# Kernel tuning notes

Hardware: AMD Instinct MI355X
Metric: run time of the kernel (lower is better)

## Reference

```python
import jax, jax.numpy as jnp
import numpy as np

N_HEADS = 16
KEY_SIZE = 64
N_INPUTS = 512
B, T = 128, 200


def setup_inputs() -> dict:
    key = jax.random.key(0)
    ks = jax.random.split(key, 6)
    s = 0.02
    return {
        "x": jax.random.normal(ks[0], (B, T, N_INPUTS), dtype=jnp.float32),
        "Wq": jax.random.normal(ks[1], (N_INPUTS, N_HEADS * KEY_SIZE), dtype=jnp.float32) * s,
        "bq": jnp.zeros((N_HEADS * KEY_SIZE,), dtype=jnp.float32),
        "Wk": jax.random.normal(ks[2], (N_INPUTS, N_HEADS * KEY_SIZE), dtype=jnp.float32) * s,
        "bk": jnp.zeros((N_HEADS * KEY_SIZE,), dtype=jnp.float32),
        "Wv": jax.random.normal(ks[3], (N_INPUTS, N_HEADS * N_INPUTS), dtype=jnp.float32) * s,
        "bv": jnp.zeros((N_HEADS * N_INPUTS,), dtype=jnp.float32),
        "Wp": jax.random.normal(ks[4], (N_HEADS * N_INPUTS, N_INPUTS), dtype=jnp.float32) * s,
        "bp": jnp.zeros((N_INPUTS,), dtype=jnp.float32),
    }


def reference(x, Wq, bq, Wk, bk, Wv, bv, Wp, bp):
    Bx, Tx, C = x.shape
    H, K = N_HEADS, KEY_SIZE
    # projections -> (B, H, T, d)
    q = (x @ Wq + bq).reshape(Bx, Tx, H, K).transpose(0, 2, 1, 3)
    k = (x @ Wk + bk).reshape(Bx, Tx, H, K).transpose(0, 2, 1, 3)
    v = (x @ Wv + bv).reshape(Bx, Tx, H, C).transpose(0, 2, 1, 3)
    scale = 1.0 / np.sqrt(K).astype(np.float32)
    scores = jnp.einsum("bhtk,bhsk->bhts", q, k) * scale  # (B,H,T,T)
    causal = jnp.tril(jnp.ones((Tx, Tx), dtype=bool))
    scores = jnp.where(causal[None, None], scores, -jnp.inf)
    att = jax.nn.softmax(scores, axis=-1)  # dropout p=0.0 (eval)
    y = jnp.einsum("bhts,bhsc->bhtc", att, v)  # (B,H,T,C)
    y = y.transpose(0, 2, 1, 3).reshape(Bx, Tx, H * C)
    return (y @ Wp + bp, att)
```

## Files before the change

### kernel.cpp

```cpp
#include <hip/hip_runtime.h>

typedef unsigned short u16;
typedef short v8s __attribute__((ext_vector_type(8)));
typedef float v4f __attribute__((ext_vector_type(4)));

#define DEV __device__ __forceinline__

constexpr int BATCH = 128;
constexpr int T = 200;
constexpr int C = 512;
constexpr int H = 16;
constexpr int BT = BATCH * T;
constexpr int TP = 208;
constexpr int TPK = 224;
constexpr int HK = 1024;
constexpr int HC = 8192;
constexpr float SCALE = 0.125f;

DEV u16 f2b(float x) {
  union { float f; unsigned u; } v; v.f = x;
  unsigned r = v.u + 0x7fffu + ((v.u >> 16) & 1u);
  return (u16)(r >> 16);
}

__global__ void cast_bf16_kernel(const float* __restrict__ in, u16* __restrict__ out, long n4) {
  long i = (long)blockIdx.x * blockDim.x + threadIdx.x;
  long stride = (long)gridDim.x * blockDim.x;
  for (; i < n4; i += stride) {
    float4 v = *(const float4*)(in + i * 4);
    uint2 o;
    o.x = (unsigned)f2b(v.x) | ((unsigned)f2b(v.y) << 16);
    o.y = (unsigned)f2b(v.z) | ((unsigned)f2b(v.w) << 16);
    *(uint2*)(out + i * 4) = o;
  }
}

__global__ void transpose_cast_kernel(const float* __restrict__ in, u16* __restrict__ out,
                                      int R, int Cc, int Rpad, long inBatch, long outBatch) {
  __shared__ float tile[32][33];
  int b = blockIdx.z;
  int c0 = blockIdx.x * 32, r0 = blockIdx.y * 32;
  int tx = threadIdx.x, ty = threadIdx.y;
  const float* ib = in + (long)b * inBatch;
  u16* ob = out + (long)b * outBatch;
  for (int i = ty; i < 32; i += 8) {
    int r = r0 + i, c = c0 + tx;
    tile[i][tx] = (r < R && c < Cc) ? ib[(long)r * Cc + c] : 0.f;
  }
  __syncthreads();
  for (int i = ty; i < 32; i += 8) {
    int c = c0 + i, r = r0 + tx;
    if (c < Cc && r < Rpad) ob[(long)c * Rpad + r] = f2b(tile[tx][i]);
  }
}

__global__ void cvec_init_kernel(const float* __restrict__ bp, float* __restrict__ cvec) {
  int j = threadIdx.x + blockIdx.x * 256;
  if (j < C) cvec[j] = bp[j];
}
__global__ void cvec_kernel(const float* __restrict__ bv, const float* __restrict__ Wp,
                            float* __restrict__ cvec) {
  int j = blockIdx.x * 256 + threadIdx.x;
  int hc0 = blockIdx.y * 256;
  float acc = 0.f;
  for (int i = 0; i < 256; i++) {
    int hc = hc0 + i;
    acc += bv[hc] * Wp[(long)hc * C + j];
  }
  atomicAdd(&cvec[j], acc);
}

template<bool OUT_BF16, bool BIAS, bool ACCUM>
__global__ __launch_bounds__(256) void gemm_nt_kernel(
    const u16* __restrict__ A, long lda, long strideA,
    const u16* __restrict__ Bt, long ldb, long strideB,
    void* __restrict__ Dp, long ldd, long strideD,
    const float* __restrict__ bias, int K, int ntN) {
  __shared__ __align__(16) u16 As[128 * 64];
  __shared__ __align__(16) u16 Bs[128 * 64];
  int bt = blockIdx.y;
  int tn = blockIdx.x % ntN, tm = blockIdx.x / ntN;
  const u16* Ab = A + (long)bt * strideA + (long)tm * 128 * lda;
  const u16* Bb = Bt + (long)bt * strideB + (long)tn * 128 * ldb;
  int tid = threadIdx.x;
  int lane = tid & 63, wave = tid >> 6;
  int r15 = lane & 15, kg = lane >> 4;
  int wm = (wave & 1) * 64, wn = (wave >> 1) * 64;
  v4f acc[4][4] = {};
  for (int kt = 0; kt < K; kt += 64) {
    uint4 va[4], vb[4];
    #pragma unroll
    for (int i = 0; i < 4; i++) {
      int c = i * 256 + tid;
      long row = c >> 3; int c8 = (c & 7) * 8;
      va[i] = *(const uint4*)(Ab + row * lda + kt + c8);
      vb[i] = *(const uint4*)(Bb + row * ldb + kt + c8);
    }
    __syncthreads();
    #pragma unroll
    for (int i = 0; i < 4; i++) {
      int c = i * 256 + tid;
      *(uint4*)(As + c * 8) = va[i];
      *(uint4*)(Bs + c * 8) = vb[i];
    }
    __syncthreads();
    #pragma unroll
    for (int ks = 0; ks < 2; ks++) {
      v8s af[4], bf_[4];
      int ko = ks * 32 + kg * 8;
      #pragma unroll
      for (int mi = 0; mi < 4; mi++) af[mi] = *(const v8s*)(As + (wm + mi * 16 + r15) * 64 + ko);
      #pragma unroll
      for (int ni = 0; ni < 4; ni++) bf_[ni] = *(const v8s*)(Bs + (wn + ni * 16 + r15) * 64 + ko);
      #pragma unroll
      for (int mi = 0; mi < 4; mi++)
        #pragma unroll
        for (int ni = 0; ni < 4; ni++)
          acc[mi][ni] = __builtin_amdgcn_mfma_f32_16x16x32_bf16(af[mi], bf_[ni], acc[mi][ni], 0, 0, 0);
    }
    __syncthreads();
  }
  #pragma unroll
  for (int mi = 0; mi < 4; mi++) {
    #pragma unroll
    for (int ni = 0; ni < 4; ni++) {
      int colg = tn * 128 + wn + ni * 16 + r15;
      float bb = BIAS ? bias[colg] : 0.f;
      #pragma unroll
      for (int r = 0; r < 4; r++) {
        long rowg = (long)tm * 128 + wm + mi * 16 + kg * 4 + r;
        long off = (long)bt * strideD + rowg * ldd + colg;
        float v = acc[mi][ni][r] + bb;
        if (OUT_BF16)      ((u16*)Dp)[off] = f2b(v);
        else if (ACCUM)    ((float*)Dp)[off] += v;
        else               ((float*)Dp)[off] = v;
      }
    }
  }
}

__global__ __launch_bounds__(256) void attn_kernel(
    const u16* __restrict__ qb, const u16* __restrict__ kb, float* __restrict__ att) {
  __shared__ __align__(16) u16 Qs[TP * 64];
  __shared__ __align__(16) u16 Ks[TP * 64];
  int bh = blockIdx.x;
  int b = bh >> 4, h = bh & 15;
  int tid = threadIdx.x;
  const u16* qg = qb + (long)b * T * HK + h * 64;
  const u16* kg_ = kb + (long)b * T * HK + h * 64;
  for (int c = tid; c < TP * 8; c += 256) {
    long row = c >> 3; int c8 = (c & 7) * 8;
    long srow = row < T ? row : (T - 1);
    *(uint4*)(Qs + c * 8) = *(const uint4*)(qg + srow * HK + c8);
    *(uint4*)(Ks + c * 8) = *(const uint4*)(kg_ + srow * HK + c8);
  }
  __syncthreads();
  int lane = tid & 63, wave = tid >> 6;
  int r15 = lane & 15, kg4 = lane >> 4;
  float* attb = att + (long)bh * T * T;
  for (int tt = wave; tt < 13; tt += 4) {
    v8s aq0 = *(const v8s*)(Qs + (tt * 16 + r15) * 64 + kg4 * 8);
    v8s aq1 = *(const v8s*)(Qs + (tt * 16 + r15) * 64 + 32 + kg4 * 8);
    float sc[13][4];
    #pragma unroll
    for (int j = 0; j < 13; j++) {
      if (j <= tt) {
        v8s bk0 = *(const v8s*)(Ks + (j * 16 + r15) * 64 + kg4 * 8);
        v8s bk1 = *(const v8s*)(Ks + (j * 16 + r15) * 64 + 32 + kg4 * 8);
        v4f a_ = {};
        a_ = __builtin_amdgcn_mfma_f32_16x16x32_bf16(aq0, bk0, a_, 0, 0, 0);
        a_ = __builtin_amdgcn_mfma_f32_16x16x32_bf16(aq1, bk1, a_, 0, 0, 0);
        #pragma unroll
        for (int r = 0; r < 4; r++) {
          int t_ = tt * 16 + kg4 * 4 + r;
          int s_ = j * 16 + r15;
          sc[j][r] = (s_ <= t_) ? a_[r] * SCALE : -__builtin_inff();
        }
      } else {
        #pragma unroll
        for (int r = 0; r < 4; r++) sc[j][r] = -__builtin_inff();
      }
    }
    float sm[4];
    #pragma unroll
    for (int r = 0; r < 4; r++) {
      float m = sc[0][r];
      #pragma unroll
      for (int j = 1; j < 13; j++) m = fmaxf(m, sc[j][r]);
      #pragma unroll
      for (int off = 1; off < 16; off <<= 1) m = fmaxf(m, __shfl_xor(m, off));
      float s = 0.f;
      #pragma unroll
      for (int j = 0; j < 13; j++) { float p = __expf(sc[j][r] - m); sc[j][r] = p; s += p; }
      #pragma unroll
      for (int off = 1; off < 16; off <<= 1) s += __shfl_xor(s, off);
      sm[r] = 1.f / s;
    }
    #pragma unroll
    for (int j = 0; j < 13; j++) {
      int s_ = j * 16 + r15;
      if (s_ < T) {
        #pragma unroll
        for (int r = 0; r < 4; r++) {
          int t_ = tt * 16 + kg4 * 4 + r;
          if (t_ < T) attb[(long)t_ * T + s_] = sc[j][r] * sm[r];
        }
      }
    }
  }
}

__global__ __launch_bounds__(256) void z_kernel(
    const float* __restrict__ att, const u16* __restrict__ xbT,
    u16* __restrict__ zb, int h0, int nhc) {
  __shared__ __align__(16) u16 As_[64 * 32];
  __shared__ __align__(16) u16 Bs_[128 * 32];
  int tt = blockIdx.x & 3, ny = blockIdx.x >> 2;
  int b = blockIdx.y / nhc, hh = blockIdx.y % nhc;
  int h = h0 + hh;
  const float* ab = att + (long)(b * H + h) * T * T;
  const u16* xg = xbT + (long)b * C * TPK;
  int tid = threadIdx.x;
  int lane = tid & 63, wave = tid >> 6;
  int r15 = lane & 15, kg4 = lane >> 4;
  int wm = (wave & 1) * 32, wn = (wave >> 1) * 64;
  v4f acc[2][4] = {};
  int ksteps = (tt + 1) * 2; if (ksteps > 7) ksteps = 7;
  int arow = tid >> 2, ac8 = (tid & 3) * 8;
  for (int ks = 0; ks < ksteps; ks++) {
    int s0 = ks * 32;
    int t_ = tt * 64 + arow;
    __align__(16) u16 tmp[8];
    #pragma unroll
    for (int e = 0; e < 8; e++) {
      int s_ = s0 + ac8 + e;
      float v = (t_ < T && s_ < T) ? ab[(long)t_ * T + s_] : 0.f;
      tmp[e] = f2b(v);
    }
    int c0 = tid, c1 = 256 + tid;
    uint4 bv0 = *(const uint4*)(xg + (long)(ny * 128 + (c0 >> 2)) * TPK + s0 + (c0 & 3) * 8);
    uint4 bv1 = *(const uint4*)(xg + (long)(ny * 128 + (c1 >> 2)) * TPK + s0 + (c1 & 3) * 8);
    __syncthreads();
    *(uint4*)(As_ + arow * 32 + ac8) = *(uint4*)tmp;
    *(uint4*)(Bs_ + c0 * 8) = bv0;
    *(uint4*)(Bs_ + c1 * 8) = bv1;
    __syncthreads();
    int ko = kg4 * 8;
    v8s a0 = *(const v8s*)(As_ + (wm + r15) * 32 + ko);
    v8s a1 = *(const v8s*)(As_ + (wm + 16 + r15) * 32 + ko);
    v8s bf_[4];
    #pragma unroll
    for (int ni = 0; ni < 4; ni++) bf_[ni] = *(const v8s*)(Bs_ + (wn + ni * 16 + r15) * 32 + ko);
    #pragma unroll
    for (int ni = 0; ni < 4; ni++) {
      acc[0][ni] = __builtin_amdgcn_mfma_f32_16x16x32_bf16(a0, bf_[ni], acc[0][ni], 0, 0, 0);
      acc[1][ni] = __builtin_amdgcn_mfma_f32_16x16x32_bf16(a1, bf_[ni], acc[1][ni], 0, 0, 0);
    }
  }
  long ldz = (long)nhc * C;
  #pragma unroll
  for (int mi = 0; mi < 2; mi++) {
    #pragma unroll
    for (int ni = 0; ni < 4; ni++) {
      int i_ = ny * 128 + wn + ni * 16 + r15;
      #pragma unroll
      for (int r = 0; r < 4; r++) {
        int t_ = tt * 64 + wm + mi * 16 + kg4 * 4 + r;
        if (t_ < T) zb[(long)(b * T + t_) * ldz + (long)hh * C + i_] = f2b(acc[mi][ni][r]);
      }
    }
  }
}

extern "C" void kernel_launch(void* const* d_in, const int* in_sizes, int n_in,
                              void* d_out, int out_size, void* d_ws, size_t ws_size,
                              hipStream_t stream) {
  const float* x  = (const float*)d_in[0];
  const float* Wq = (const float*)d_in[1];
  const float* bq = (const float*)d_in[2];
  const float* Wk = (const float*)d_in[3];
  const float* bk = (const float*)d_in[4];
  const float* Wv = (const float*)d_in[5];
  const float* bv = (const float*)d_in[6];
  const float* Wp = (const float*)d_in[7];
  const float* bp = (const float*)d_in[8];
  float* out = (float*)d_out;
  float* att = out + (long)BT * C;

  char* w = (char*)d_ws;
  auto alloc = [&](size_t bytes) -> char* {
    char* p = w; w += (bytes + 255) & ~(size_t)255; return p;
  };
  u16* xb  = (u16*)alloc((size_t)BT * C * 2);
  u16* xbT = (u16*)alloc((size_t)BATCH * C * TPK * 2);
  u16* qb  = (u16*)alloc((size_t)BT * HK * 2);
  u16* kb  = (u16*)alloc((size_t)BT * HK * 2);
  u16* wqT = (u16*)alloc((size_t)HK * C * 2);
  u16* wkT = (u16*)alloc((size_t)HK * C * 2);
  u16* wvb = (u16*)alloc((size_t)C * HC * 2);
  u16* wpT = (u16*)alloc((size_t)C * HC * 2);
  u16* w2t = (u16*)alloc((size_t)C * HC * 2);
  float* cv = (float*)alloc(C * 4);
  size_t used = (size_t)(w - (char*)d_ws);
  size_t rem = ws_size > used ? ws_size - used : 0;
  int nhc = 16;
  while (nhc > 1 && (size_t)BT * nhc * C * 2 > rem) nhc >>= 1;
  u16* zb = (u16*)alloc((size_t)BT * nhc * C * 2);

  cast_bf16_kernel<<<2048, 256, 0, stream>>>(x, xb, (long)BT * C / 4);
  cast_bf16_kernel<<<2048, 256, 0, stream>>>(Wv, wvb, (long)C * HC / 4);
  dim3 tb(32, 8);
  transpose_cast_kernel<<<dim3(C / 32, TPK / 32, BATCH), tb, 0, stream>>>(x, xbT, T, C, TPK, (long)T * C, (long)C * TPK);
  transpose_cast_kernel<<<dim3(HK / 32, C / 32, 1), tb, 0, stream>>>(Wq, wqT, C, HK, C, 0, 0);
  transpose_cast_kernel<<<dim3(HK / 32, C / 32, 1), tb, 0, stream>>>(Wk, wkT, C, HK, C, 0, 0);
  transpose_cast_kernel<<<dim3(C / 32, HC / 32, 1), tb, 0, stream>>>(Wp, wpT, HC, C, HC, 0, 0);
  cvec_init_kernel<<<2, 256, 0, stream>>>(bp, cv);
  cvec_kernel<<<dim3(2, 32), 256, 0, stream>>>(bv, Wp, cv);
  gemm_nt_kernel<true, true, false><<<dim3(200 * 8, 1), 256, 0, stream>>>(
      xb, C, 0, wqT, C, 0, qb, HK, 0, bq, C, 8);
  gemm_nt_kernel<true, true, false><<<dim3(200 * 8, 1), 256, 0, stream>>>(
      xb, C, 0, wkT, C, 0, kb, HK, 0, bk, C, 8);
  gemm_nt_kernel<true, false, false><<<dim3(16, H), 256, 0, stream>>>(
      wpT, HC, C, wvb, HC, C, w2t, HC, C, nullptr, C, 4);
  attn_kernel<<<dim3(BATCH * H), 256, 0, stream>>>(qb, kb, att);
  int nch = H / nhc;
  for (int cc = 0; cc < nch; cc++) {
    z_kernel<<<dim3(16, BATCH * nhc), 256, 0, stream>>>(att, xbT, zb, cc * nhc, nhc);
    if (cc == 0)
      gemm_nt_kernel<false, true, false><<<dim3(200 * 4, 1), 256, 0, stream>>>(
          zb, (long)nhc * C, 0, w2t + (long)cc * nhc * C, HC, 0, out, C, 0, cv, nhc * C, 4);
    else
      gemm_nt_kernel<false, false, true><<<dim3(200 * 4, 1), 256, 0, stream>>>(
          zb, (long)nhc * C, 0, w2t + (long)cc * nhc * C, HC, 0, out, C, 0, nullptr, nhc * C, 4);
  }
}
```

Baseline: 2.848 ms.

## Reassociate output path: project x through fused Wv·Wp before attention weighting

Instead of computing z = att·x per head and then multiplying by the fused Wv·Wp matrix, the code first computes y2 = x·(Wv_h·Wp) per head (stored transposed, padded per batch), then a new out_kernel accumulates att_h·y2_h over all heads directly into the output with the bias vector. This removes the per-head zb intermediate and the separate final GEMM with accumulation passes, and drops the transposed x copy. In exchange it materialises a large per-batch HC×TPK bf16 buffer, chunked by batch depending on workspace, and out_kernel loops serially over 16 heads per block, which concentrates the work in a small grid.

Result: faster. 2.513 ms (-11.8%).

```diff
diff --git a/kernel.cpp b/kernel.cpp
--- a/kernel.cpp
+++ b/kernel.cpp
@@ -70,7 +70,7 @@
   atomicAdd(&cvec[j], acc);
 }
 
-template<bool OUT_BF16, bool BIAS, bool ACCUM>
+template<bool OUT_BF16, bool BIAS, bool ACCUM, bool Y2T>
 __global__ __launch_bounds__(256) void gemm_nt_kernel(
     const u16* __restrict__ A, long lda, long strideA,
     const u16* __restrict__ Bt, long ldb, long strideB,
@@ -129,11 +129,16 @@
       #pragma unroll
       for (int r = 0; r < 4; r++) {
         long rowg = (long)tm * 128 + wm + mi * 16 + kg * 4 + r;
-        long off = (long)bt * strideD + rowg * ldd + colg;
         float v = acc[mi][ni][r] + bb;
-        if (OUT_BF16)      ((u16*)Dp)[off] = f2b(v);
-        else if (ACCUM)    ((float*)Dp)[off] += v;
-        else               ((float*)Dp)[off] = v;
+        if (Y2T) {
+          int b2 = colg / T; int ss = colg - b2 * T;
+          ((u16*)Dp)[((long)b2 * HC + rowg) * TPK + ss] = f2b(v);
+        } else {
+          long off = (long)bt * strideD + rowg * ldd + colg;
+          if (OUT_BF16)      ((u16*)Dp)[off] = f2b(v);
+          else if (ACCUM)    ((float*)Dp)[off] += v;
+          else               ((float*)Dp)[off] = v;
+        }
       }
     }
   }
@@ -210,63 +215,70 @@
   }
 }
 
-__global__ __launch_bounds__(256) void z_kernel(
-    const float* __restrict__ att, const u16* __restrict__ xbT,
-    u16* __restrict__ zb, int h0, int nhc) {
-  __shared__ __align__(16) u16 As_[64 * 32];
+__global__ __launch_bounds__(256) void out_kernel(
+    const float* __restrict__ att, const u16* __restrict__ y2t,
+    const float* __restrict__ cvec, float* __restrict__ out) {
+  __shared__ __align__(16) u16 As_[128 * 32];
   __shared__ __align__(16) u16 Bs_[128 * 32];
-  int tt = blockIdx.x & 3, ny = blockIdx.x >> 2;
-  int b = blockIdx.y / nhc, hh = blockIdx.y % nhc;
-  int h = h0 + hh;
-  const float* ab = att + (long)(b * H + h) * T * T;
-  const u16* xg = xbT + (long)b * C * TPK;
+  int bx = blockIdx.x;
+  int mt = bx >> 2, tn = bx & 3;
+  int b = blockIdx.y;
+  int t0 = mt * 128;
+  const float* ab = att + (long)b * H * T * T;
+  const u16* yb = y2t + (long)b * HC * TPK;
   int tid = threadIdx.x;
   int lane = tid & 63, wave = tid >> 6;
   int r15 = lane & 15, kg4 = lane >> 4;
-  int wm = (wave & 1) * 32, wn = (wave >> 1) * 64;
-  v4f acc[2][4] = {};
-  int ksteps = (tt + 1) * 2; if (ksteps > 7) ksteps = 7;
-  int arow = tid >> 2, ac8 = (tid & 3) * 8;
-  for (int ks = 0; ks < ksteps; ks++) {
-    int s0 = ks * 32;
-    int t_ = tt * 64 + arow;
-    __align__(16) u16 tmp[8];
-    #pragma unroll
-    for (int e = 0; e < 8; e++) {
-      int s_ = s0 + ac8 + e;
-      float v = (t_ < T && s_ < T) ? ab[(long)t_ * T + s_] : 0.f;
-      tmp[e] = f2b(v);
-    }
-    int c0 = tid, c1 = 256 + tid;
-    uint4 bv0 = *(const uint4*)(xg + (long)(ny * 128 + (c0 >> 2)) * TPK + s0 + (c0 & 3) * 8);
-    uint4 bv1 = *(const uint4*)(xg + (long)(ny * 128 + (c1 >> 2)) * TPK + s0 + (c1 & 3) * 8);
-    __syncthreads();
-    *(uint4*)(As_ + arow * 32 + ac8) = *(uint4*)tmp;
-    *(uint4*)(Bs_ + c0 * 8) = bv0;
-    *(uint4*)(Bs_ + c1 * 8) = bv1;
-    __syncthreads();
-    int ko = kg4 * 8;
-    v8s a0 = *(const v8s*)(As_ + (wm + r15) * 32 + ko);
-    v8s a1 = *(const v8s*)(As_ + (wm + 16 + r15) * 32 + ko);
-    v8s bf_[4];
-    #pragma unroll
-    for (int ni = 0; ni < 4; ni++) bf_[ni] = *(const v8s*)(Bs_ + (wn + ni * 16 + r15) * 32 + ko);
+  int wm = (wave & 1) * 64, wn = (wave >> 1) * 64;
+  int arow = tid >> 1, ac = (tid & 1) * 16;
+  v4f acc[4][4] = {};
+  int nsc = (t0 == 0) ? 4 : 7;
+  for (int h = 0; h < H; h++) {
+    const float* ah = ab + (long)h * T * T;
+    const u16* yh = yb + (long)(h * C + tn * 128) * TPK;
+    for (int sc = 0; sc < nsc; sc++) {
+      int s0 = sc * 32;
+      int t_ = t0 + arow;
+      __align__(16) u16 ta[16];
+      #pragma unroll
+      for (int e = 0; e < 16; e++) {
+        int s_ = s0 + ac + e;
+        float v = 0.f;
+        if (t_ < T && s_ < T) v = ah[(long)t_ * T + s_];
+        ta[e] = f2b(v);
+      }
+      uint4 bv0 = *(const uint4*)(yh + (long)arow * TPK + s0 + ac);
+      uint4 bv1 = *(const uint4*)(yh + (long)arow * TPK + s0 + ac + 8);
+      __syncthreads();
+      *(uint4*)(As_ + arow * 32 + ac) = *(uint4*)ta;
+      *(uint4*)(As_ + arow * 32 + ac + 8) = *(uint4*)(ta + 8);
+      *(uint4*)(Bs_ + arow * 32 + ac) = bv0;
+      *(uint4*)(Bs_ + arow * 32 + ac + 8) = bv1;
+      __syncthreads();
+      int ko = kg4 * 8;
+      v8s af[4], bf_[4];
+      #pragma unroll
+      for (int mi = 0; mi < 4; mi++) af[mi] = *(const v8s*)(As_ + (wm + mi * 16 + r15) * 32 + ko);
+      #pragma unroll
+      for (int ni = 0; ni < 4; ni++) bf_[ni] = *(const v8s*)(Bs_ + (wn + ni * 16 + r15) * 32 + ko);
+      #pragma unroll
+      for (int mi = 0; mi < 4; mi++)
+        #pragma unroll
+        for (int ni = 0; ni < 4; ni++)
+          acc[mi][ni] = __builtin_amdgcn_mfma_f32_16x16x32_bf16(af[mi], bf_[ni], acc[mi][ni], 0, 0, 0);
+      __syncthreads();
+    }
+  }
+  #pragma unroll
+  for (int mi = 0; mi < 4; mi++) {
     #pragma unroll
     for (int ni = 0; ni < 4; ni++) {
-      acc[0][ni] = __builtin_amdgcn_mfma_f32_16x16x32_bf16(a0, bf_[ni], acc[0][ni], 0, 0, 0);
-      acc[1][ni] = __builtin_amdgcn_mfma_f32_16x16x32_bf16(a1, bf_[ni], acc[1][ni], 0, 0, 0);
-    }
-  }
-  long ldz = (long)nhc * C;
-  #pragma unroll
-  for (int mi = 0; mi < 2; mi++) {
-    #pragma unroll
-    for (int ni = 0; ni < 4; ni++) {
-      int i_ = ny * 128 + wn + ni * 16 + r15;
+      int colg = tn * 128 + wn + ni * 16 + r15;
+      float bb = cvec[colg];
       #pragma unroll
       for (int r = 0; r < 4; r++) {
-        int t_ = tt * 64 + wm + mi * 16 + kg4 * 4 + r;
-        if (t_ < T) zb[(long)(b * T + t_) * ldz + (long)hh * C + i_] = f2b(acc[mi][ni][r]);
+        int t_ = t0 + wm + mi * 16 + kg4 * 4 + r;
+        if (t_ < T) out[((long)b * T + t_) * C + colg] = acc[mi][ni][r] + bb;
       }
     }
   }
@@ -292,45 +304,41 @@
     char* p = w; w += (bytes + 255) & ~(size_t)255; return p;
   };
   u16* xb  = (u16*)alloc((size_t)BT * C * 2);
-  u16* xbT = (u16*)alloc((size_t)BATCH * C * TPK * 2);
   u16* qb  = (u16*)alloc((size_t)BT * HK * 2);
   u16* kb  = (u16*)alloc((size_t)BT * HK * 2);
   u16* wqT = (u16*)alloc((size_t)HK * C * 2);
   u16* wkT = (u16*)alloc((size_t)HK * C * 2);
+  u16* w2n = (u16*)alloc((size_t)HC * C * 2);
+  float* cv = (float*)alloc(C * 4);
+  char* scratch0 = w;
   u16* wvb = (u16*)alloc((size_t)C * HC * 2);
-  u16* wpT = (u16*)alloc((size_t)C * HC * 2);
-  u16* w2t = (u16*)alloc((size_t)C * HC * 2);
-  float* cv = (float*)alloc(C * 4);
-  size_t used = (size_t)(w - (char*)d_ws);
-  size_t rem = ws_size > used ? ws_size - used : 0;
-  int nhc = 16;
-  while (nhc > 1 && (size_t)BT * nhc * C * 2 > rem) nhc >>= 1;
-  u16* zb = (u16*)alloc((size_t)BT * nhc * C * 2);
+  u16* wpT = (u16*)alloc((size_t)HC * C * 2);
+  u16* y2t = (u16*)scratch0;
+  size_t rem = ws_size > (size_t)(scratch0 - (char*)d_ws)
+             ? ws_size - (size_t)(scratch0 - (char*)d_ws) : 0;
+  int nbc = 128;
+  while (nbc > 16 && (size_t)nbc * HC * TPK * 2 > rem) nbc >>= 1;
 
   cast_bf16_kernel<<<2048, 256, 0, stream>>>(x, xb, (long)BT * C / 4);
   cast_bf16_kernel<<<2048, 256, 0, stream>>>(Wv, wvb, (long)C * HC / 4);
   dim3 tb(32, 8);
-  transpose_cast_kernel<<<dim3(C / 32, TPK / 32, BATCH), tb, 0, stream>>>(x, xbT, T, C, TPK, (long)T * C, (long)C * TPK);
   transpose_cast_kernel<<<dim3(HK / 32, C / 32, 1), tb, 0, stream>>>(Wq, wqT, C, HK, C, 0, 0);
   transpose_cast_kernel<<<dim3(HK / 32, C / 32, 1), tb, 0, stream>>>(Wk, wkT, C, HK, C, 0, 0);
   transpose_cast_kernel<<<dim3(C / 32, HC / 32, 1), tb, 0, stream>>>(Wp, wpT, HC, C, HC, 0, 0);
   cvec_init_kernel<<<2, 256, 0, stream>>>(bp, cv);
   cvec_kernel<<<dim3(2, 32), 256, 0, stream>>>(bv, Wp, cv);
-  gemm_nt_kernel<true, true, false><<<dim3(200 * 8, 1), 256, 0, stream>>>(
+  gemm_nt_kernel<true, true, false, false><<<dim3(200 * 8, 1), 256, 0, stream>>>(
       xb, C, 0, wqT, C, 0, qb, HK, 0, bq, C, 8);
-  gemm_nt_kernel<true, true, false><<<dim3(200 * 8, 1), 256, 0, stream>>>(
+  gemm_nt_kernel<true, true, false, false><<<dim3(200 * 8, 1), 256, 0, stream>>>(
       xb, C, 0, wkT, C, 0, kb, HK, 0, bk, C, 8);
-  gemm_nt_kernel<true, false, false><<<dim3(16, H), 256, 0, stream>>>(
-      wpT, HC, C, wvb, HC, C, w2t, HC, C, nullptr, C, 4);
+  gemm_nt_kernel<true, false, false, false><<<dim3(16, H), 256, 0, stream>>>(
+      wpT, HC, C, wvb, HC, C, w2n, C, (long)C * C, nullptr, C, 4);
   attn_kernel<<<dim3(BATCH * H), 256, 0, stream>>>(qb, kb, att);
-  int nch = H / nhc;
-  for (int cc = 0; cc < nch; cc++) {
-    z_kernel<<<dim3(16, BATCH * nhc), 256, 0, stream>>>(att, xbT, zb, cc * nhc, nhc);
-    if (cc == 0)
-      gemm_nt_kernel<false, true, false><<<dim3(200 * 4, 1), 256, 0, stream>>>(
-          zb, (long)nhc * C, 0, w2t + (long)cc * nhc * C, HC, 0, out, C, 0, cv, nhc * C, 4);
-    else
-      gemm_nt_kernel<false, false, true><<<dim3(200 * 4, 1), 256, 0, stream>>>(
-          zb, (long)nhc * C, 0, w2t + (long)cc * nhc * C, HC, 0, out, C, 0, nullptr, nhc * C, 4);
-  }
-}
+  for (int b0 = 0; b0 < BATCH; b0 += nbc) {
+    int ntn = nbc * T / 128;
+    gemm_nt_kernel<false, false, false, true><<<dim3(64 * ntn, 1), 256, 0, stream>>>(
+        w2n, C, 0, xb + (long)b0 * T * C, C, 0, y2t, 0, 0, nullptr, C, ntn);
+    out_kernel<<<dim3(8, nbc), 256, 0, stream>>>(
+        att + (long)b0 * H * T * T, y2t, cv, out + (long)b0 * T * C);
+  }
+}
```
